# Optimization experiments

Hardware: AMD Instinct MI355X
Metric: run time of the kernel (lower is better)

## Reference

```python
import jax, jax.numpy as jnp
import numpy as np

N_NODES = 50000
N_EDGES = 600000
D = 128
HIDDEN = 128
N_GRAPHS = 128
N_CLASSES = 10
N_STACKED = 3  # num_layers - 1


def setup_inputs() -> dict:
    key = jax.random.key(0)
    ks = jax.random.split(key, 12)
    s = 1.0 / np.sqrt(HIDDEN)
    inp = {
        "x": jax.random.normal(ks[0], (N_NODES, D), dtype=jnp.float32),
        "edge_index": jax.random.randint(ks[1], (2, N_EDGES), 0, N_NODES, dtype=jnp.int64),
        "batch": jnp.sort(jax.random.randint(ks[2], (N_NODES,), 0, N_GRAPHS, dtype=jnp.int64)),
        "W1": jax.random.normal(ks[3], (D, HIDDEN), dtype=jnp.float32) * s,
        "R1": jax.random.normal(ks[4], (D, HIDDEN), dtype=jnp.float32) * s,
        "b1": jnp.zeros((HIDDEN,), dtype=jnp.float32),
        "Wc": jax.random.normal(ks[5], (N_STACKED, HIDDEN, HIDDEN), dtype=jnp.float32) * s,
        "Rc": jax.random.normal(ks[6], (N_STACKED, HIDDEN, HIDDEN), dtype=jnp.float32) * s,
        "bc": jnp.zeros((N_STACKED, HIDDEN), dtype=jnp.float32),
        "lin1_w": jax.random.normal(ks[7], (HIDDEN, HIDDEN), dtype=jnp.float32) * s,
        "lin1_b": jnp.zeros((HIDDEN,), dtype=jnp.float32),
        "lin2_w": jax.random.normal(ks[8], (HIDDEN, N_CLASSES), dtype=jnp.float32) * s,
        "lin2_b": jnp.zeros((N_CLASSES,), dtype=jnp.float32),
    }
    return inp


def _gcn_norm(edge_index, n_nodes):
    # symmetric GCN normalization coeffs per edge (edge_weight=None -> ones)
    src, dst = edge_index[0], edge_index[1]
    ones = jnp.ones((edge_index.shape[1],), dtype=jnp.float32)
    deg = jax.ops.segment_sum(ones, dst, num_segments=n_nodes)
    dinv = jnp.where(deg > 0, jax.lax.rsqrt(jnp.maximum(deg, 1.0)), 0.0)
    return dinv[src] * dinv[dst]


def _gcs(x, src, dst, norm, W, R, b):
    # GCN aggregation on transformed features + linear skip (root) connection
    h = x @ W                                   # [N, H]
    msg = h[src] * norm[:, None]                # gather + scale, [E, H]
    agg = jax.ops.segment_sum(msg, dst, num_segments=x.shape[0])
    return agg + x @ R + b


def reference(x, edge_index, batch, W1, R1, b1, Wc, Rc, bc,
              lin1_w, lin1_b, lin2_w, lin2_b):
    src, dst = edge_index[0], edge_index[1]
    norm = _gcn_norm(edge_index, x.shape[0])

    h = jax.nn.relu(_gcs(x, src, dst, norm, W1, R1, b1))
    for i in range(N_STACKED):
        h = jax.nn.relu(_gcs(h, src, dst, norm, Wc[i], Rc[i], bc[i]))
    last = h

    # global mean pool over graphs
    sums = jax.ops.segment_sum(h, batch, num_segments=N_GRAPHS)
    cnts = jax.ops.segment_sum(jnp.ones((h.shape[0],), h.dtype), batch,
                               num_segments=N_GRAPHS)
    pooled = sums / jnp.maximum(cnts, 1.0)[:, None]

    g = jax.nn.relu(pooled @ lin1_w + lin1_b)   # dropout is identity in eval mode
    logits = g @ lin2_w + lin2_b
    return jax.nn.log_softmax(logits, axis=-1), last
```

## Files before the change

### kernel.cpp

```cpp
#include <hip/hip_runtime.h>

#define N_NODES  50000
#define N_EDGES  600000
#define DIM      128
#define N_GRAPHS 128
#define N_CLASSES 10
#define NB_SCAN  196
#define ZWORDS   1700000
#define NZB4     1661
#define NPB      16


typedef __bf16 bf16x8 __attribute__((ext_vector_type(8)));
typedef float  f32x4  __attribute__((ext_vector_type(4)));

__device__ inline unsigned short f2bf(float f) {
  union { float f; unsigned int i; } u; u.f = f;
  unsigned int r = u.i + 0x7fff + ((u.i >> 16) & 1);
  return (unsigned short)(r >> 16);
}
__device__ inline float bf2f(unsigned short s) {
  union { unsigned int i; float f; } u; u.i = ((unsigned int)s) << 16;
  return u.f;
}
__device__ inline bf16x8 pack8(float4 lo, float4 hi) {
  union { bf16x8 v; unsigned short s[8]; } u;
  u.s[0] = f2bf(lo.x); u.s[1] = f2bf(lo.y); u.s[2] = f2bf(lo.z); u.s[3] = f2bf(lo.w);
  u.s[4] = f2bf(hi.x); u.s[5] = f2bf(hi.y); u.s[6] = f2bf(hi.z); u.s[7] = f2bf(hi.w);
  return u.v;
}
__device__ inline bf16x8 zero8() {
  union { bf16x8 v; unsigned short s[8]; } u;
#pragma unroll
  for (int j = 0; j < 8; ++j) u.s[j] = 0;
  return u.v;
}


__global__ __launch_bounds__(256) void k_prep(float4* __restrict__ z4,
                                              float4* __restrict__ pz,
                                              const float* __restrict__ W1,
                                              const float* __restrict__ R1,
                                              const float* __restrict__ Wc,
                                              const float* __restrict__ Rc,
                                              unsigned short* __restrict__ pk) {
  if (blockIdx.x < NZB4) {
    int i = blockIdx.x * 256 + threadIdx.x;
    if (i < ZWORDS / 4) z4[i] = make_float4(0.f, 0.f, 0.f, 0.f);
    return;
  }
  if (blockIdx.x < NZB4 + NPB) {
    int i = (blockIdx.x - NZB4) * 256 + threadIdx.x;
    pz[i] = make_float4(0.f, 0.f, 0.f, 0.f);
    return;
  }
  int pb = blockIdx.x - NZB4 - NPB;
  int mm = pb >> 3, sub = pb & 7;
  const float* src = (mm == 0) ? W1
                   : (mm < 4)  ? Wc + (size_t)(mm - 1) * DIM * DIM
                   : (mm == 4) ? R1
                               : Rc + (size_t)(mm - 5) * DIM * DIM;
  int idx = sub * 256 + threadIdx.x;
  int lane = idx & 63;
  int kc   = (idx >> 6) & 3;
  int nt   = idx >> 8;
  int col  = nt * 16 + (lane & 15);
  int k0   = kc * 32 + (lane >> 4) * 8;
  unsigned short* dst = pk + (size_t)mm * 16384 + (size_t)idx * 8;
  ushort4 u;
  u.x = f2bf(src[(k0 + 0) * DIM + col]);
  u.y = f2bf(src[(k0 + 1) * DIM + col]);
  u.z = f2bf(src[(k0 + 2) * DIM + col]);
  u.w = f2bf(src[(k0 + 3) * DIM + col]);
  *(ushort4*)&dst[0] = u;
  u.x = f2bf(src[(k0 + 4) * DIM + col]);
  u.y = f2bf(src[(k0 + 5) * DIM + col]);
  u.z = f2bf(src[(k0 + 6) * DIM + col]);
  u.w = f2bf(src[(k0 + 7) * DIM + col]);
  *(ushort4*)&dst[4] = u;
}


__global__ __launch_bounds__(256) void k_deg(const int* __restrict__ ei,
                                             int* __restrict__ deg) {
  int e = blockIdx.x * 256 + threadIdx.x;
  if (e < N_EDGES) atomicAdd(&deg[ei[N_EDGES + e]], 1);
}

__global__ __launch_bounds__(256) void k_dinvsum(const int* __restrict__ deg,
                                                 float* __restrict__ dinv,
                                                 int* __restrict__ bsum) {
  int i = blockIdx.x * 256 + threadIdx.x;
  int t = threadIdx.x;
  int d = (i < N_NODES) ? deg[i] : 0;
  if (i < N_NODES) dinv[i] = (d > 0) ? rsqrtf((float)d) : 0.f;
  int dp = (d + 7) & ~7;
  __shared__ int tmp[256];
  tmp[t] = dp;
  __syncthreads();
  for (int off = 128; off > 0; off >>= 1) {
    if (t < off) tmp[t] += tmp[t + off];
    __syncthreads();
  }
  if (t == 0) bsum[blockIdx.x] = tmp[0];
}

__global__ __launch_bounds__(256) void k_bscan(const int* __restrict__ bsum,
                                               int* __restrict__ boff,
                                               int* __restrict__ rowp) {
  int t = threadIdx.x;
  int v = (t < NB_SCAN) ? bsum[t] : 0;
  __shared__ int tmp[256];
  tmp[t] = v;
  __syncthreads();
  for (int off = 1; off < 256; off <<= 1) {
    int add = (t >= off) ? tmp[t - off] : 0;
    __syncthreads();
    tmp[t] += add;
    __syncthreads();
  }
  boff[t] = tmp[t] - v;
  if (t == 255) rowp[N_NODES] = tmp[255];
}

__global__ __launch_bounds__(256) void k_rowp(const int* __restrict__ deg,
                                              const int* __restrict__ boff,
                                              int* __restrict__ rowp) {
  int i = blockIdx.x * 256 + threadIdx.x;
  int t = threadIdx.x;
  int dp = (i < N_NODES) ? ((deg[i] + 7) & ~7) : 0;
  __shared__ int tmp[256];
  tmp[t] = dp;
  __syncthreads();
  for (int off = 1; off < 256; off <<= 1) {
    int add = (t >= off) ? tmp[t - off] : 0;
    __syncthreads();
    tmp[t] += add;
    __syncthreads();
  }
  if (i < N_NODES) rowp[i] = boff[blockIdx.x] + tmp[t] - dp;
}

__global__ __launch_bounds__(256) void k_fill(const int* __restrict__ ei,
                                              const int* __restrict__ rowp,
                                              int* __restrict__ cnt,
                                              const float* __restrict__ dinv,
                                              int2* __restrict__ epk) {
  int e = blockIdx.x * 256 + threadIdx.x;
  if (e < N_EDGES) {
    int s = ei[e];
    int d = ei[N_EDGES + e];
    int p = rowp[d] + atomicAdd(&cnt[d], 1);
    epk[p] = make_int2(s, __float_as_int(dinv[s] * dinv[d]));
  }
}


__global__ __launch_bounds__(256) void k_gemm0(const float* __restrict__ xf,
                                               const unsigned short* __restrict__ pkW,
                                               const unsigned short* __restrict__ pkR,
                                               const float* __restrict__ bv,
                                               unsigned short* __restrict__ hwb,
                                               unsigned short* __restrict__ skipb) {
  const int tid  = threadIdx.x;
  const int wave = tid >> 6, lane = tid & 63;
  const int m = lane & 15, q = lane >> 4;
  const int rbase = blockIdx.x * 64 + wave * 16;
  const int arow  = rbase + m;
  const bool aok  = arow < N_NODES;

  bf16x8 a[4];
#pragma unroll
  for (int kc = 0; kc < 4; ++kc) {
    float4 lo = make_float4(0.f, 0.f, 0.f, 0.f);
    float4 hi = make_float4(0.f, 0.f, 0.f, 0.f);
    if (aok) {
      lo = *(const float4*)&xf[arow * DIM + kc * 32 + q * 8];
      hi = *(const float4*)&xf[arow * DIM + kc * 32 + q * 8 + 4];
    }
    a[kc] = pack8(lo, hi);
  }

  f32x4 acc[16];
#pragma unroll
  for (int t = 0; t < 16; ++t) acc[t] = (f32x4){0.f, 0.f, 0.f, 0.f};

#pragma unroll
  for (int nt = 0; nt < 8; ++nt) {
    const unsigned short* pw = pkW + ((size_t)(nt * 4) * 64 + lane) * 8;
    const unsigned short* pr = pkR + ((size_t)(nt * 4) * 64 + lane) * 8;
#pragma unroll
    for (int kc = 0; kc < 4; ++kc) {
      bf16x8 bW = *(const bf16x8*)(pw + (size_t)kc * 64 * 8);
      acc[nt] = __builtin_amdgcn_mfma_f32_16x16x32_bf16(a[kc], bW, acc[nt], 0, 0, 0);
    }
#pragma unroll
    for (int kc = 0; kc < 4; ++kc) {
      bf16x8 bR = *(const bf16x8*)(pr + (size_t)kc * 64 * 8);
      acc[8 + nt] = __builtin_amdgcn_mfma_f32_16x16x32_bf16(a[kc], bR, acc[8 + nt], 0, 0, 0);
    }
  }

#pragma unroll
  for (int nt = 0; nt < 8; ++nt) {
    int col = nt * 16 + m;
    float bias = bv[col];
#pragma unroll
    for (int rg = 0; rg < 4; ++rg) {
      int row = rbase + q * 4 + rg;
      if (row < N_NODES) {
        hwb[row * DIM + col]   = f2bf(acc[nt][rg]);
        skipb[row * DIM + col] = f2bf(acc[8 + nt][rg] + bias);
      }
    }
  }
}


__global__ __launch_bounds__(256) void k_gath(const unsigned short* __restrict__ hin,
                                              const int* __restrict__ rowp,
                                              const int2* __restrict__ epk,
                                              const unsigned short* __restrict__ skipb,
                                              unsigned short* __restrict__ gout) {
  int n = blockIdx.x * 8 + (threadIdx.x >> 5);
  if (n >= N_NODES) return;
  int l4 = (threadIdx.x & 31) * 4;
  int e0 = rowp[n], e1 = rowp[n + 1];
  ushort4 s = *(const ushort4*)&skipb[n * DIM + l4];
  float4 accA = make_float4(0.f, 0.f, 0.f, 0.f);
  float4 accB = make_float4(0.f, 0.f, 0.f, 0.f);
  for (int ea = e0, eb = e1 - 4; ea < eb; ea += 4, eb -= 4) {
    int4 p0 = *(const int4*)&epk[ea];
    int4 p1 = *(const int4*)&epk[ea + 2];
    int4 p2 = *(const int4*)&epk[eb];
    int4 p3 = *(const int4*)&epk[eb + 2];
    ushort4 u0 = *(const ushort4*)&hin[p0.x * DIM + l4];
    ushort4 u1 = *(const ushort4*)&hin[p0.z * DIM + l4];
    ushort4 u2 = *(const ushort4*)&hin[p1.x * DIM + l4];
    ushort4 u3 = *(const ushort4*)&hin[p1.z * DIM + l4];
    ushort4 u4 = *(const ushort4*)&hin[p2.x * DIM + l4];
    ushort4 u5 = *(const ushort4*)&hin[p2.z * DIM + l4];
    ushort4 u6 = *(const ushort4*)&hin[p3.x * DIM + l4];
    ushort4 u7 = *(const ushort4*)&hin[p3.z * DIM + l4];
    float w0 = __int_as_float(p0.y), w1 = __int_as_float(p0.w);
    float w2 = __int_as_float(p1.y), w3 = __int_as_float(p1.w);
    float w4 = __int_as_float(p2.y), w5 = __int_as_float(p2.w);
    float w6 = __int_as_float(p3.y), w7 = __int_as_float(p3.w);
    accA.x = fmaf(w0, bf2f(u0.x), fmaf(w1, bf2f(u1.x), fmaf(w2, bf2f(u2.x), fmaf(w3, bf2f(u3.x), accA.x))));
    accA.y = fmaf(w0, bf2f(u0.y), fmaf(w1, bf2f(u1.y), fmaf(w2, bf2f(u2.y), fmaf(w3, bf2f(u3.y), accA.y))));
    accA.z = fmaf(w0, bf2f(u0.z), fmaf(w1, bf2f(u1.z), fmaf(w2, bf2f(u2.z), fmaf(w3, bf2f(u3.z), accA.z))));
    accA.w = fmaf(w0, bf2f(u0.w), fmaf(w1, bf2f(u1.w), fmaf(w2, bf2f(u2.w), fmaf(w3, bf2f(u3.w), accA.w))));
    accB.x = fmaf(w4, bf2f(u4.x), fmaf(w5, bf2f(u5.x), fmaf(w6, bf2f(u6.x), fmaf(w7, bf2f(u7.x), accB.x))));
    accB.y = fmaf(w4, bf2f(u4.y), fmaf(w5, bf2f(u5.y), fmaf(w6, bf2f(u6.y), fmaf(w7, bf2f(u7.y), accB.y))));
    accB.z = fmaf(w4, bf2f(u4.z), fmaf(w5, bf2f(u5.z), fmaf(w6, bf2f(u6.z), fmaf(w7, bf2f(u7.z), accB.z))));
    accB.w = fmaf(w4, bf2f(u4.w), fmaf(w5, bf2f(u5.w), fmaf(w6, bf2f(u6.w), fmaf(w7, bf2f(u7.w), accB.w))));
  }
  ushort4 o;
  o.x = f2bf(fmaxf(accA.x + accB.x + bf2f(s.x), 0.f));
  o.y = f2bf(fmaxf(accA.y + accB.y + bf2f(s.y), 0.f));
  o.z = f2bf(fmaxf(accA.z + accB.z + bf2f(s.z), 0.f));
  o.w = f2bf(fmaxf(accA.w + accB.w + bf2f(s.w), 0.f));
  *(ushort4*)&gout[n * DIM + l4] = o;
}


template<bool LAST>
__global__ __launch_bounds__(256) void k_gemmb(unsigned short* __restrict__ gio,
                                               const unsigned short* __restrict__ pkW,
                                               const unsigned short* __restrict__ pkR,
                                               const float* __restrict__ bv,
                                               unsigned short* __restrict__ skipb,
                                               float* __restrict__ skipf) {
  const int tid  = threadIdx.x;
  const int wave = tid >> 6, lane = tid & 63;
  const int m = lane & 15, q = lane >> 4;
  const int rbase = blockIdx.x * 64 + wave * 16;
  const int arow  = rbase + m;
  const bool aok  = arow < N_NODES;

  bf16x8 a[4];
#pragma unroll
  for (int kc = 0; kc < 4; ++kc)
    a[kc] = aok ? *(const bf16x8*)&gio[arow * DIM + kc * 32 + q * 8] : zero8();

  f32x4 acc[16];
#pragma unroll
  for (int t = 0; t < 16; ++t) acc[t] = (f32x4){0.f, 0.f, 0.f, 0.f};

#pragma unroll
  for (int nt = 0; nt < 8; ++nt) {
    const unsigned short* pw = pkW + ((size_t)(nt * 4) * 64 + lane) * 8;
    const unsigned short* pr = pkR + ((size_t)(nt * 4) * 64 + lane) * 8;
#pragma unroll
    for (int kc = 0; kc < 4; ++kc) {
      bf16x8 bW = *(const bf16x8*)(pw + (size_t)kc * 64 * 8);
      acc[nt] = __builtin_amdgcn_mfma_f32_16x16x32_bf16(a[kc], bW, acc[nt], 0, 0, 0);
    }
#pragma unroll
    for (int kc = 0; kc < 4; ++kc) {
      bf16x8 bR = *(const bf16x8*)(pr + (size_t)kc * 64 * 8);
      acc[8 + nt] = __builtin_amdgcn_mfma_f32_16x16x32_bf16(a[kc], bR, acc[8 + nt], 0, 0, 0);
    }
  }

#pragma unroll
  for (int nt = 0; nt < 8; ++nt) {
    int col = nt * 16 + m;
    float bias = bv[col];
#pragma unroll
    for (int rg = 0; rg < 4; ++rg) {
      int row = rbase + q * 4 + rg;
      if (row < N_NODES) {
        gio[row * DIM + col] = f2bf(acc[nt][rg]);
        float v = acc[8 + nt][rg] + bias;
        if (LAST) skipf[row * DIM + col] = v;
        else      skipb[row * DIM + col] = f2bf(v);
      }
    }
  }
}


__global__ __launch_bounds__(256) void k_aggF(const unsigned short* __restrict__ hwb,
                                              const int* __restrict__ rowp,
                                              const int2* __restrict__ epk,
                                              const int* __restrict__ batch,
                                              float* __restrict__ actf,
                                              float* __restrict__ psum) {
  __shared__ float sp[8][132];
  __shared__ int gb[8];
  const int tid = threadIdx.x;
  const int n0 = blockIdx.x * 8;
  const int n = n0 + (tid >> 5);
  const int l4 = (tid & 31) * 4;
  if (tid < 8) gb[tid] = batch[n0 + tid];
  int e0 = rowp[n], e1 = rowp[n + 1];
  float4 s = *(const float4*)&actf[n * DIM + l4];
  float4 accA = make_float4(0.f, 0.f, 0.f, 0.f);
  float4 accB = make_float4(0.f, 0.f, 0.f, 0.f);
  for (int ea = e0, eb = e1 - 4; ea < eb; ea += 4, eb -= 4) {
    int4 p0 = *(const int4*)&epk[ea];
    int4 p1 = *(const int4*)&epk[ea + 2];
    int4 p2 = *(const int4*)&epk[eb];
    int4 p3 = *(const int4*)&epk[eb + 2];
    ushort4 u0 = *(const ushort4*)&hwb[p0.x * DIM + l4];
    ushort4 u1 = *(const ushort4*)&hwb[p0.z * DIM + l4];
    ushort4 u2 = *(const ushort4*)&hwb[p1.x * DIM + l4];
    ushort4 u3 = *(const ushort4*)&hwb[p1.z * DIM + l4];
    ushort4 u4 = *(const ushort4*)&hwb[p2.x * DIM + l4];
    ushort4 u5 = *(const ushort4*)&hwb[p2.z * DIM + l4];
    ushort4 u6 = *(const ushort4*)&hwb[p3.x * DIM + l4];
    ushort4 u7 = *(const ushort4*)&hwb[p3.z * DIM + l4];
    float w0 = __int_as_float(p0.y), w1 = __int_as_float(p0.w);
    float w2 = __int_as_float(p1.y), w3 = __int_as_float(p1.w);
    float w4 = __int_as_float(p2.y), w5 = __int_as_float(p2.w);
    float w6 = __int_as_float(p3.y), w7 = __int_as_float(p3.w);
    accA.x = fmaf(w0, bf2f(u0.x), fmaf(w1, bf2f(u1.x), fmaf(w2, bf2f(u2.x), fmaf(w3, bf2f(u3.x), accA.x))));
    accA.y = fmaf(w0, bf2f(u0.y), fmaf(w1, bf2f(u1.y), fmaf(w2, bf2f(u2.y), fmaf(w3, bf2f(u3.y), accA.y))));
    accA.z = fmaf(w0, bf2f(u0.z), fmaf(w1, bf2f(u1.z), fmaf(w2, bf2f(u2.z), fmaf(w3, bf2f(u3.z), accA.z))));
    accA.w = fmaf(w0, bf2f(u0.w), fmaf(w1, bf2f(u1.w), fmaf(w2, bf2f(u2.w), fmaf(w3, bf2f(u3.w), accA.w))));
    accB.x = fmaf(w4, bf2f(u4.x), fmaf(w5, bf2f(u5.x), fmaf(w6, bf2f(u6.x), fmaf(w7, bf2f(u7.x), accB.x))));
    accB.y = fmaf(w4, bf2f(u4.y), fmaf(w5, bf2f(u5.y), fmaf(w6, bf2f(u6.y), fmaf(w7, bf2f(u7.y), accB.y))));
    accB.z = fmaf(w4, bf2f(u4.z), fmaf(w5, bf2f(u5.z), fmaf(w6, bf2f(u6.z), fmaf(w7, bf2f(u7.z), accB.z))));
    accB.w = fmaf(w4, bf2f(u4.w), fmaf(w5, bf2f(u5.w), fmaf(w6, bf2f(u6.w), fmaf(w7, bf2f(u7.w), accB.w))));
  }
  float4 o;
  o.x = fmaxf(accA.x + accB.x + s.x, 0.f);
  o.y = fmaxf(accA.y + accB.y + s.y, 0.f);
  o.z = fmaxf(accA.z + accB.z + s.z, 0.f);
  o.w = fmaxf(accA.w + accB.w + s.w, 0.f);
  *(float4*)&actf[n * DIM + l4] = o;
  int r = tid >> 5;
  sp[r][l4 + 0] = o.x; sp[r][l4 + 1] = o.y;
  sp[r][l4 + 2] = o.z; sp[r][l4 + 3] = o.w;
  __syncthreads();
  if (tid < DIM) {
    int gprev = gb[0];
    float acc = 0.f;
#pragma unroll
    for (int rr = 0; rr < 8; ++rr) {
      int g = gb[rr];
      if (g != gprev) { atomicAdd(&psum[gprev * DIM + tid], acc); acc = 0.f; gprev = g; }
      acc += sp[rr][tid];
    }
    atomicAdd(&psum[gprev * DIM + tid], acc);
  }
}


__global__ __launch_bounds__(128) void k_mlp1(const float* __restrict__ psum,
                                              const int* __restrict__ batch,
                                              const float* __restrict__ w,
                                              const float* __restrict__ bias,
                                              float* __restrict__ g1) {
  int g = blockIdx.x, t = threadIdx.x;
  __shared__ int sb[2];
  if (t < 2) {
    int target = g + t;
    int lo = 0, hi = N_NODES;
    while (lo < hi) {
      int mid = (lo + hi) >> 1;
      if (batch[mid] < target) lo = mid + 1; else hi = mid;
    }
    sb[t] = lo;
  }
  __syncthreads();
  float cnt = fmaxf((float)(sb[1] - sb[0]), 1.f);
  __shared__ float sp[DIM];
  sp[t] = psum[g * DIM + t] / cnt;
  __syncthreads();
  float acc = bias[t];
#pragma unroll 4
  for (int k = 0; k < DIM; ++k) acc = fmaf(sp[k], w[k * DIM + t], acc);
  g1[g * DIM + t] = fmaxf(acc, 0.f);
}

__global__ __launch_bounds__(128) void k_mlp2(const float* __restrict__ g1,
                                              const float* __restrict__ w,
                                              const float* __restrict__ bias,
                                              float* __restrict__ out) {
  int g = threadIdx.x;
  float l[N_CLASSES];
#pragma unroll
  for (int c = 0; c < N_CLASSES; ++c) l[c] = bias[c];
  for (int k = 0; k < DIM; ++k) {
    float gv = g1[g * DIM + k];
#pragma unroll
    for (int c = 0; c < N_CLASSES; ++c) l[c] = fmaf(gv, w[k * N_CLASSES + c], l[c]);
  }
  float m = l[0];
#pragma unroll
  for (int c = 1; c < N_CLASSES; ++c) m = fmaxf(m, l[c]);
  float s = 0.f;
#pragma unroll
  for (int c = 0; c < N_CLASSES; ++c) s += expf(l[c] - m);
  float lse = logf(s) + m;
#pragma unroll
  for (int c = 0; c < N_CLASSES; ++c) out[g * N_CLASSES + c] = l[c] - lse;
}


extern "C" void kernel_launch(void* const* d_in, const int* in_sizes, int n_in,
                              void* d_out, int out_size, void* d_ws, size_t ws_size,
                              hipStream_t stream) {
  const float* x     = (const float*)d_in[0];
  const int* ei      = (const int*)d_in[1];
  const int* batch   = (const int*)d_in[2];
  const float* W1  = (const float*)d_in[3];
  const float* R1  = (const float*)d_in[4];
  const float* b1  = (const float*)d_in[5];
  const float* Wc  = (const float*)d_in[6];
  const float* Rc  = (const float*)d_in[7];
  const float* bc  = (const float*)d_in[8];
  const float* l1w = (const float*)d_in[9];
  const float* l1b = (const float*)d_in[10];
  const float* l2w = (const float*)d_in[11];
  const float* l2b = (const float*)d_in[12];

  float* out   = (float*)d_out;
  float* dlast = out + N_GRAPHS * N_CLASSES;

  float* ws = (float*)d_ws;
  unsigned short* X = (unsigned short*)ws;
  unsigned short* Y = (unsigned short*)(ws + 3203072);
  unsigned short* S = (unsigned short*)(ws + 6406144);
  int*   deg   = (int*)(ws + 9609216);
  int*   cnt   = (int*)(ws + 9659216);
  int2*  epk   = (int2*)(ws + 9709216);
  float* dinv  = ws + 11309216;
  int*   rowp  = (int*)(ws + 11359216);
  float* psum  = ws + 11409232;
  float* g1    = ws + 11425616;
  unsigned short* pk = (unsigned short*)(ws + 11442000);
  int*   bsum  = (int*)(ws + 11507536);
  int*   boff  = (int*)(ws + 11507792);

  k_prep<<<NZB4 + NPB + 64, 256, 0, stream>>>((float4*)(ws + 9609216),
                                              (float4*)psum, W1, R1, Wc, Rc, pk);
  k_deg <<<(N_EDGES + 255) / 256, 256, 0, stream>>>(ei, deg);
  k_dinvsum<<<NB_SCAN, 256, 0, stream>>>(deg, dinv, bsum);
  k_bscan<<<1, 256, 0, stream>>>(bsum, boff, rowp);
  k_rowp<<<NB_SCAN, 256, 0, stream>>>(deg, boff, rowp);
  k_fill<<<(N_EDGES + 255) / 256, 256, 0, stream>>>(ei, rowp, cnt, dinv, epk);

  const int NGB = (N_NODES + 63) / 64;
  const int NAB = (N_NODES + 7) / 8;

  k_gemm0<<<NGB, 256, 0, stream>>>(x, pk + 0 * 16384, pk + 4 * 16384, b1, X, S);
  k_gath <<<NAB, 256, 0, stream>>>(X, rowp, epk, S, Y);
  k_gemmb<false><<<NGB, 256, 0, stream>>>(Y, pk + 1 * 16384, pk + 5 * 16384,
                                          bc + 0 * DIM, S, nullptr);
  k_gath <<<NAB, 256, 0, stream>>>(Y, rowp, epk, S, X);
  k_gemmb<false><<<NGB, 256, 0, stream>>>(X, pk + 2 * 16384, pk + 6 * 16384,
                                          bc + 1 * DIM, S, nullptr);
  k_gath <<<NAB, 256, 0, stream>>>(X, rowp, epk, S, Y);
  k_gemmb<true><<<NGB, 256, 0, stream>>>(Y, pk + 3 * 16384, pk + 7 * 16384,
                                         bc + 2 * DIM, S, dlast);
  k_aggF<<<NAB, 256, 0, stream>>>(Y, rowp, epk, batch, dlast, psum);

  k_mlp1<<<N_GRAPHS, 128, 0, stream>>>(psum, batch, l1w, l1b, g1);
  k_mlp2<<<1, N_GRAPHS, 0, stream>>>(g1, l2w, l2b, out);
}
```

Measured before the change: 372.2 us.

## Aggregate before transform: gather raw features, then fuse both GEMMs with ReLU and pooling

Reorders each GCN layer from transform-then-aggregate to aggregate-then-transform, using A(XW) = (AX)W. Each layer now gathers bf16 node features and then runs one GEMM kernel that multiplies the aggregated features by W and the input by R, adding bias and applying ReLU. The last layer's GEMM also writes the fp32 output and does the mean-pool partial sums, which removes the separate k_aggF pass and the intermediate skip buffer writes and reads. It adds a standalone x-to-bf16 cast kernel, and the gather of raw bf16 input features changes where rounding happens.

```diff
diff --git a/kernel.cpp b/kernel.cpp
--- a/kernel.cpp
+++ b/kernel.cpp
@@ -156,77 +156,24 @@
 }
 
 
-__global__ __launch_bounds__(256) void k_gemm0(const float* __restrict__ xf,
-                                               const unsigned short* __restrict__ pkW,
-                                               const unsigned short* __restrict__ pkR,
-                                               const float* __restrict__ bv,
-                                               unsigned short* __restrict__ hwb,
-                                               unsigned short* __restrict__ skipb) {
-  const int tid  = threadIdx.x;
-  const int wave = tid >> 6, lane = tid & 63;
-  const int m = lane & 15, q = lane >> 4;
-  const int rbase = blockIdx.x * 64 + wave * 16;
-  const int arow  = rbase + m;
-  const bool aok  = arow < N_NODES;
-
-  bf16x8 a[4];
-#pragma unroll
-  for (int kc = 0; kc < 4; ++kc) {
-    float4 lo = make_float4(0.f, 0.f, 0.f, 0.f);
-    float4 hi = make_float4(0.f, 0.f, 0.f, 0.f);
-    if (aok) {
-      lo = *(const float4*)&xf[arow * DIM + kc * 32 + q * 8];
-      hi = *(const float4*)&xf[arow * DIM + kc * 32 + q * 8 + 4];
-    }
-    a[kc] = pack8(lo, hi);
-  }
-
-  f32x4 acc[16];
-#pragma unroll
-  for (int t = 0; t < 16; ++t) acc[t] = (f32x4){0.f, 0.f, 0.f, 0.f};
-
-#pragma unroll
-  for (int nt = 0; nt < 8; ++nt) {
-    const unsigned short* pw = pkW + ((size_t)(nt * 4) * 64 + lane) * 8;
-    const unsigned short* pr = pkR + ((size_t)(nt * 4) * 64 + lane) * 8;
-#pragma unroll
-    for (int kc = 0; kc < 4; ++kc) {
-      bf16x8 bW = *(const bf16x8*)(pw + (size_t)kc * 64 * 8);
-      acc[nt] = __builtin_amdgcn_mfma_f32_16x16x32_bf16(a[kc], bW, acc[nt], 0, 0, 0);
-    }
-#pragma unroll
-    for (int kc = 0; kc < 4; ++kc) {
-      bf16x8 bR = *(const bf16x8*)(pr + (size_t)kc * 64 * 8);
-      acc[8 + nt] = __builtin_amdgcn_mfma_f32_16x16x32_bf16(a[kc], bR, acc[8 + nt], 0, 0, 0);
-    }
-  }
-
-#pragma unroll
-  for (int nt = 0; nt < 8; ++nt) {
-    int col = nt * 16 + m;
-    float bias = bv[col];
-#pragma unroll
-    for (int rg = 0; rg < 4; ++rg) {
-      int row = rbase + q * 4 + rg;
-      if (row < N_NODES) {
-        hwb[row * DIM + col]   = f2bf(acc[nt][rg]);
-        skipb[row * DIM + col] = f2bf(acc[8 + nt][rg] + bias);
-      }
-    }
-  }
+__global__ __launch_bounds__(256) void k_xcast(const float* __restrict__ xf,
+                                               unsigned short* __restrict__ xb) {
+  int i = blockIdx.x * 256 + threadIdx.x;
+  float4 lo = *(const float4*)&xf[i * 8];
+  float4 hi = *(const float4*)&xf[i * 8 + 4];
+  bf16x8 v = pack8(lo, hi);
+  *(bf16x8*)&xb[i * 8] = v;
 }
 
 
 __global__ __launch_bounds__(256) void k_gath(const unsigned short* __restrict__ hin,
                                               const int* __restrict__ rowp,
                                               const int2* __restrict__ epk,
-                                              const unsigned short* __restrict__ skipb,
-                                              unsigned short* __restrict__ gout) {
+                                              unsigned short* __restrict__ aout) {
   int n = blockIdx.x * 8 + (threadIdx.x >> 5);
   if (n >= N_NODES) return;
   int l4 = (threadIdx.x & 31) * 4;
   int e0 = rowp[n], e1 = rowp[n + 1];
-  ushort4 s = *(const ushort4*)&skipb[n * DIM + l4];
   float4 accA = make_float4(0.f, 0.f, 0.f, 0.f);
   float4 accB = make_float4(0.f, 0.f, 0.f, 0.f);
   for (int ea = e0, eb = e1 - 4; ea < eb; ea += 4, eb -= 4) {
@@ -256,32 +203,38 @@
     accB.w = fmaf(w4, bf2f(u4.w), fmaf(w5, bf2f(u5.w), fmaf(w6, bf2f(u6.w), fmaf(w7, bf2f(u7.w), accB.w))));
   }
   ushort4 o;
-  o.x = f2bf(fmaxf(accA.x + accB.x + bf2f(s.x), 0.f));
-  o.y = f2bf(fmaxf(accA.y + accB.y + bf2f(s.y), 0.f));
-  o.z = f2bf(fmaxf(accA.z + accB.z + bf2f(s.z), 0.f));
-  o.w = f2bf(fmaxf(accA.w + accB.w + bf2f(s.w), 0.f));
-  *(ushort4*)&gout[n * DIM + l4] = o;
+  o.x = f2bf(accA.x + accB.x);
+  o.y = f2bf(accA.y + accB.y);
+  o.z = f2bf(accA.z + accB.z);
+  o.w = f2bf(accA.w + accB.w);
+  *(ushort4*)&aout[n * DIM + l4] = o;
 }
 
 
 template<bool LAST>
-__global__ __launch_bounds__(256) void k_gemmb(unsigned short* __restrict__ gio,
+__global__ __launch_bounds__(256) void k_gemmc(const unsigned short* __restrict__ aA,
+                                               const unsigned short* __restrict__ gA,
                                                const unsigned short* __restrict__ pkW,
                                                const unsigned short* __restrict__ pkR,
                                                const float* __restrict__ bv,
-                                               unsigned short* __restrict__ skipb,
-                                               float* __restrict__ skipf) {
+                                               unsigned short* __restrict__ gout,
+                                               float* __restrict__ dlast,
+                                               const int* __restrict__ batch,
+                                               float* __restrict__ psum) {
   const int tid  = threadIdx.x;
   const int wave = tid >> 6, lane = tid & 63;
   const int m = lane & 15, q = lane >> 4;
-  const int rbase = blockIdx.x * 64 + wave * 16;
-  const int arow  = rbase + m;
-  const bool aok  = arow < N_NODES;
-
-  bf16x8 a[4];
-#pragma unroll
-  for (int kc = 0; kc < 4; ++kc)
-    a[kc] = aok ? *(const bf16x8*)&gio[arow * DIM + kc * 32 + q * 8] : zero8();
+  const int rbase0 = blockIdx.x * 64;
+  const int rbase  = rbase0 + wave * 16;
+  const int arow   = rbase + m;
+  const bool aok   = arow < N_NODES;
+
+  bf16x8 a[4], g[4];
+#pragma unroll
+  for (int kc = 0; kc < 4; ++kc) {
+    a[kc] = aok ? *(const bf16x8*)&aA[arow * DIM + kc * 32 + q * 8] : zero8();
+    g[kc] = aok ? *(const bf16x8*)&gA[arow * DIM + kc * 32 + q * 8] : zero8();
+  }
 
   f32x4 acc[16];
 #pragma unroll
@@ -299,91 +252,50 @@
 #pragma unroll
     for (int kc = 0; kc < 4; ++kc) {
       bf16x8 bR = *(const bf16x8*)(pr + (size_t)kc * 64 * 8);
-      acc[8 + nt] = __builtin_amdgcn_mfma_f32_16x16x32_bf16(a[kc], bR, acc[8 + nt], 0, 0, 0);
-    }
-  }
-
-#pragma unroll
-  for (int nt = 0; nt < 8; ++nt) {
-    int col = nt * 16 + m;
-    float bias = bv[col];
-#pragma unroll
-    for (int rg = 0; rg < 4; ++rg) {
-      int row = rbase + q * 4 + rg;
-      if (row < N_NODES) {
-        gio[row * DIM + col] = f2bf(acc[nt][rg]);
-        float v = acc[8 + nt][rg] + bias;
-        if (LAST) skipf[row * DIM + col] = v;
-        else      skipb[row * DIM + col] = f2bf(v);
+      acc[8 + nt] = __builtin_amdgcn_mfma_f32_16x16x32_bf16(g[kc], bR, acc[8 + nt], 0, 0, 0);
+    }
+  }
+
+  if constexpr (!LAST) {
+#pragma unroll
+    for (int nt = 0; nt < 8; ++nt) {
+      int col = nt * 16 + m;
+      float bias = bv[col];
+#pragma unroll
+      for (int rg = 0; rg < 4; ++rg) {
+        int row = rbase + q * 4 + rg;
+        if (row < N_NODES)
+          gout[row * DIM + col] = f2bf(fmaxf(acc[nt][rg] + acc[8 + nt][rg] + bias, 0.f));
       }
     }
-  }
-}
-
-
-__global__ __launch_bounds__(256) void k_aggF(const unsigned short* __restrict__ hwb,
-                                              const int* __restrict__ rowp,
-                                              const int2* __restrict__ epk,
-                                              const int* __restrict__ batch,
-                                              float* __restrict__ actf,
-                                              float* __restrict__ psum) {
-  __shared__ float sp[8][132];
-  __shared__ int gb[8];
-  const int tid = threadIdx.x;
-  const int n0 = blockIdx.x * 8;
-  const int n = n0 + (tid >> 5);
-  const int l4 = (tid & 31) * 4;
-  if (tid < 8) gb[tid] = batch[n0 + tid];
-  int e0 = rowp[n], e1 = rowp[n + 1];
-  float4 s = *(const float4*)&actf[n * DIM + l4];
-  float4 accA = make_float4(0.f, 0.f, 0.f, 0.f);
-  float4 accB = make_float4(0.f, 0.f, 0.f, 0.f);
-  for (int ea = e0, eb = e1 - 4; ea < eb; ea += 4, eb -= 4) {
-    int4 p0 = *(const int4*)&epk[ea];
-    int4 p1 = *(const int4*)&epk[ea + 2];
-    int4 p2 = *(const int4*)&epk[eb];
-    int4 p3 = *(const int4*)&epk[eb + 2];
-    ushort4 u0 = *(const ushort4*)&hwb[p0.x * DIM + l4];
-    ushort4 u1 = *(const ushort4*)&hwb[p0.z * DIM + l4];
-    ushort4 u2 = *(const ushort4*)&hwb[p1.x * DIM + l4];
-    ushort4 u3 = *(const ushort4*)&hwb[p1.z * DIM + l4];
-    ushort4 u4 = *(const ushort4*)&hwb[p2.x * DIM + l4];
-    ushort4 u5 = *(const ushort4*)&hwb[p2.z * DIM + l4];
-    ushort4 u6 = *(const ushort4*)&hwb[p3.x * DIM + l4];
-    ushort4 u7 = *(const ushort4*)&hwb[p3.z * DIM + l4];
-    float w0 = __int_as_float(p0.y), w1 = __int_as_float(p0.w);
-    float w2 = __int_as_float(p1.y), w3 = __int_as_float(p1.w);
-    float w4 = __int_as_float(p2.y), w5 = __int_as_float(p2.w);
-    float w6 = __int_as_float(p3.y), w7 = __int_as_float(p3.w);
-    accA.x = fmaf(w0, bf2f(u0.x), fmaf(w1, bf2f(u1.x), fmaf(w2, bf2f(u2.x), fmaf(w3, bf2f(u3.x), accA.x))));
-    accA.y = fmaf(w0, bf2f(u0.y), fmaf(w1, bf2f(u1.y), fmaf(w2, bf2f(u2.y), fmaf(w3, bf2f(u3.y), accA.y))));
-    accA.z = fmaf(w0, bf2f(u0.z), fmaf(w1, bf2f(u1.z), fmaf(w2, bf2f(u2.z), fmaf(w3, bf2f(u3.z), accA.z))));
-    accA.w = fmaf(w0, bf2f(u0.w), fmaf(w1, bf2f(u1.w), fmaf(w2, bf2f(u2.w), fmaf(w3, bf2f(u3.w), accA.w))));
-    accB.x = fmaf(w4, bf2f(u4.x), fmaf(w5, bf2f(u5.x), fmaf(w6, bf2f(u6.x), fmaf(w7, bf2f(u7.x), accB.x))));
-    accB.y = fmaf(w4, bf2f(u4.y), fmaf(w5, bf2f(u5.y), fmaf(w6, bf2f(u6.y), fmaf(w7, bf2f(u7.y), accB.y))));
-    accB.z = fmaf(w4, bf2f(u4.z), fmaf(w5, bf2f(u5.z), fmaf(w6, bf2f(u6.z), fmaf(w7, bf2f(u7.z), accB.z))));
-    accB.w = fmaf(w4, bf2f(u4.w), fmaf(w5, bf2f(u5.w), fmaf(w6, bf2f(u6.w), fmaf(w7, bf2f(u7.w), accB.w))));
-  }
-  float4 o;
-  o.x = fmaxf(accA.x + accB.x + s.x, 0.f);
-  o.y = fmaxf(accA.y + accB.y + s.y, 0.f);
-  o.z = fmaxf(accA.z + accB.z + s.z, 0.f);
-  o.w = fmaxf(accA.w + accB.w + s.w, 0.f);
-  *(float4*)&actf[n * DIM + l4] = o;
-  int r = tid >> 5;
-  sp[r][l4 + 0] = o.x; sp[r][l4 + 1] = o.y;
-  sp[r][l4 + 2] = o.z; sp[r][l4 + 3] = o.w;
-  __syncthreads();
-  if (tid < DIM) {
-    int gprev = gb[0];
-    float acc = 0.f;
-#pragma unroll
-    for (int rr = 0; rr < 8; ++rr) {
-      int g = gb[rr];
-      if (g != gprev) { atomicAdd(&psum[gprev * DIM + tid], acc); acc = 0.f; gprev = g; }
-      acc += sp[rr][tid];
-    }
-    atomicAdd(&psum[gprev * DIM + tid], acc);
+  } else {
+    __shared__ float sp[64][132];
+    __shared__ int gb[64];
+    if (tid < 64) gb[tid] = batch[min(rbase0 + tid, N_NODES - 1)];
+#pragma unroll
+    for (int nt = 0; nt < 8; ++nt) {
+      int col = nt * 16 + m;
+      float bias = bv[col];
+#pragma unroll
+      for (int rg = 0; rg < 4; ++rg) {
+        int r   = wave * 16 + q * 4 + rg;
+        int row = rbase0 + r;
+        float v = fmaxf(acc[nt][rg] + acc[8 + nt][rg] + bias, 0.f);
+        if (row < N_NODES) dlast[row * DIM + col] = v;
+        sp[r][col] = (row < N_NODES) ? v : 0.f;
+      }
+    }
+    __syncthreads();
+    if (tid < DIM) {
+      int gprev = gb[0];
+      float acc2 = 0.f;
+      for (int rr = 0; rr < 64; ++rr) {
+        int gg = gb[rr];
+        if (gg != gprev) { atomicAdd(&psum[gprev * DIM + tid], acc2); acc2 = 0.f; gprev = gg; }
+        acc2 += sp[rr][tid];
+      }
+      atomicAdd(&psum[gprev * DIM + tid], acc2);
+    }
   }
 }
 
@@ -486,17 +398,19 @@
   const int NGB = (N_NODES + 63) / 64;
   const int NAB = (N_NODES + 7) / 8;
 
-  k_gemm0<<<NGB, 256, 0, stream>>>(x, pk + 0 * 16384, pk + 4 * 16384, b1, X, S);
-  k_gath <<<NAB, 256, 0, stream>>>(X, rowp, epk, S, Y);
-  k_gemmb<false><<<NGB, 256, 0, stream>>>(Y, pk + 1 * 16384, pk + 5 * 16384,
-                                          bc + 0 * DIM, S, nullptr);
-  k_gath <<<NAB, 256, 0, stream>>>(Y, rowp, epk, S, X);
-  k_gemmb<false><<<NGB, 256, 0, stream>>>(X, pk + 2 * 16384, pk + 6 * 16384,
-                                          bc + 1 * DIM, S, nullptr);
-  k_gath <<<NAB, 256, 0, stream>>>(X, rowp, epk, S, Y);
-  k_gemmb<true><<<NGB, 256, 0, stream>>>(Y, pk + 3 * 16384, pk + 7 * 16384,
-                                         bc + 2 * DIM, S, dlast);
-  k_aggF<<<NAB, 256, 0, stream>>>(Y, rowp, epk, batch, dlast, psum);
+  k_xcast<<<3125, 256, 0, stream>>>(x, X);
+  k_gath <<<NAB, 256, 0, stream>>>(X, rowp, epk, S);
+  k_gemmc<false><<<NGB, 256, 0, stream>>>(S, X, pk + 0 * 16384, pk + 4 * 16384,
+                                          b1, Y, nullptr, nullptr, nullptr);
+  k_gath <<<NAB, 256, 0, stream>>>(Y, rowp, epk, S);
+  k_gemmc<false><<<NGB, 256, 0, stream>>>(S, Y, pk + 1 * 16384, pk + 5 * 16384,
+                                          bc + 0 * DIM, X, nullptr, nullptr, nullptr);
+  k_gath <<<NAB, 256, 0, stream>>>(X, rowp, epk, S);
+  k_gemmc<false><<<NGB, 256, 0, stream>>>(S, X, pk + 2 * 16384, pk + 6 * 16384,
+                                          bc + 1 * DIM, Y, nullptr, nullptr, nullptr);
+  k_gath <<<NAB, 256, 0, stream>>>(Y, rowp, epk, S);
+  k_gemmc<true><<<NGB, 256, 0, stream>>>(S, Y, pk + 3 * 16384, pk + 7 * 16384,
+                                         bc + 2 * DIM, nullptr, dlast, batch, psum);
 
   k_mlp1<<<N_GRAPHS, 128, 0, stream>>>(psum, batch, l1w, l1b, g1);
   k_mlp2<<<1, N_GRAPHS, 0, stream>>>(g1, l2w, l2b, out);
```

Result: no change. 370.3 us (median of 2 runs) (-0.5%).
